# Optimization experiments

Hardware: AMD Instinct MI355X
Metric: run time of the kernel (lower is better)

## Reference

```python
import jax, jax.numpy as jnp
import numpy as np

B, N, D, C, H, W = 4, 900, 256, 256, 200, 200
HEADS, LVLS, PTS, K = 8, 1, 4, 10


def setup_inputs() -> dict:
    key = jax.random.key(0)
    ks = jax.random.split(key, 16)
    s = 0.02
    return {
        "query_embed": jax.random.normal(ks[0], (B, N, D), jnp.float32),
        "ctrl_points": jax.random.uniform(ks[1], (B, N, 4, 2), jnp.float32, -50.0, 50.0),
        "bev_features": jax.random.normal(ks[2], (B, C, H, W), jnp.float32),
        "spatial_shapes": jnp.array([[H, W]], dtype=jnp.int32),
        "pc_range": jnp.array([-51.2, -51.2, -5.0, 51.2, 51.2, 3.0], jnp.float32),
        "Wq": s * jax.random.normal(ks[3], (D, D)), "bq": jnp.zeros((D,)),
        "Wv": s * jax.random.normal(ks[4], (C, D)), "bv": jnp.zeros((D,)),
        "Woff": s * jax.random.normal(ks[5], (D, HEADS * LVLS * PTS * 2)), "boff": jnp.zeros((HEADS * LVLS * PTS * 2,)),
        "Wattn": s * jax.random.normal(ks[6], (D, HEADS * LVLS * PTS)), "battn": jnp.zeros((HEADS * LVLS * PTS,)),
        "Wmo": s * jax.random.normal(ks[7], (D, D)), "bmo": jnp.zeros((D,)),
        "Wo": s * jax.random.normal(ks[8], (D, D)), "bo": jnp.zeros((D,)),
    }


def _forward(query_embed, ctrl_points, bev_features, spatial_shapes, pc_range,
             Wq, bq, Wv, bv, Woff, boff, Wattn, battn, Wmo, bmo, Wo, bo):
    b, n, d = query_embed.shape
    _, c, h, w = bev_features.shape
    hd = d // HEADS

    # --- cubic Bezier interpolation: (B,N,4,2) -> (B,N,K,2) dense points ---
    t = jnp.linspace(0.0, 1.0, K, dtype=query_embed.dtype)
    basis = jnp.stack([(1 - t) ** 3, 3 * (1 - t) ** 2 * t, 3 * (1 - t) * t ** 2, t ** 3], axis=-1)  # (K,4)
    dense = jnp.einsum('kc,bncd->bnkd', basis, ctrl_points)
    # --- normalize to [0,1] by pc_range, clamp to [0.01,0.99] ---
    nx = (dense[..., 0] - pc_range[0]) / (pc_range[3] - pc_range[0])
    ny = (dense[..., 1] - pc_range[1]) / (pc_range[4] - pc_range[1])
    ref = jnp.clip(jnp.stack([nx, ny], axis=-1), 0.01, 0.99)  # (B,N,K,2)

    # --- projections ---
    q = query_embed @ Wq + bq                                       # (B,N,D) (identity for residual)
    v = bev_features.reshape(b, c, h * w).transpose(0, 2, 1) @ Wv + bv  # (B,HW,D)
    v = v.reshape(b, h * w, HEADS, hd)

    off = (q @ Woff + boff).reshape(b, n, HEADS, LVLS, PTS, 2)
    aw = jax.nn.softmax((q @ Wattn + battn).reshape(b, n, HEADS, LVLS * PTS), axis=-1)
    aw = aw.reshape(b, n, HEADS, PTS)  # LVLS == 1

    # offset normalizer = (W, H) per level
    normalizer = jnp.stack([spatial_shapes[..., 1], spatial_shapes[..., 0]], axis=-1).astype(q.dtype)  # (L,2)
    # sampling locations: broadcast K bezier points against heads/points offsets
    loc = ref[:, :, None, :, None, :] + off / normalizer[None, None, None, :, None, :]  # (B,N,HEADS,K,PTS,2)

    # --- bilinear sampling, align_corners=False, zero padding ---
    gx = loc[..., 0] * w - 0.5
    gy = loc[..., 1] * h - 0.5
    x0 = jnp.floor(gx)
    y0 = jnp.floor(gy)
    wx = gx - x0
    wy = gy - y0
    x0i = x0.astype(jnp.int32)
    y0i = y0.astype(jnp.int32)

    vflat = v.transpose(0, 2, 1, 3).reshape(b * HEADS, h * w, hd)  # (B*HEADS, HW, hd)

    def flat(a):  # (B,N,HEADS,K,PTS) -> (B*HEADS, N*K*PTS)
        return a.transpose(0, 2, 1, 3, 4).reshape(b * HEADS, n * K * PTS)

    acc = jnp.zeros((b * HEADS, n * K * PTS, hd), dtype=q.dtype)
    for dx, dy in ((0, 0), (1, 0), (0, 1), (1, 1)):
        ix = flat(x0i) + dx
        iy = flat(y0i) + dy
        wxx = flat(wx) if dx else (1.0 - flat(wx))
        wyy = flat(wy) if dy else (1.0 - flat(wy))
        valid = (ix >= 0) & (ix < w) & (iy >= 0) & (iy < h)
        idx = jnp.clip(iy, 0, h - 1) * w + jnp.clip(ix, 0, w - 1)
        corner = jnp.take_along_axis(vflat, idx[..., None], axis=1)  # (B*HEADS, Npts, hd)
        acc = acc + corner * (wxx * wyy * valid.astype(q.dtype))[..., None]

    sampled = acc.reshape(b, HEADS, n, K, PTS, hd)
    # weighted sum over (K, PTS); attention weights shared across the K bezier points
    out = jnp.einsum('bhnkpd,bnhp->bnhd', sampled, aw).reshape(b, n, d)
    out = out @ Wmo + bmo + q   # mmcv MSDeformAttn output_proj + residual (identity = query)
    out = out @ Wo + bo         # outer output_proj
    return out


def reference(query_embed, ctrl_points, bev_features, spatial_shapes, pc_range,
              Wq, bq, Wv, bv, Woff, boff, Wattn, battn, Wmo, bmo, Wo, bo):
    return _forward(query_embed, ctrl_points, bev_features, spatial_shapes, pc_range,
                    Wq, bq, Wv, bv, Woff, boff, Wattn, battn, Wmo, bmo, Wo, bo)
```

## Files before the change

kernel.cpp:

```cpp
#include <hip/hip_runtime.h>
#include <hip/hip_bf16.h>
#include <math.h>


typedef unsigned short u16;
typedef unsigned int u32;
typedef short bf16x8 __attribute__((ext_vector_type(8)));
typedef float f32x4 __attribute__((ext_vector_type(4)));

__device__ __forceinline__ float bflo(u32 w) {
  union { u32 i; float f; } c; c.i = w << 16; return c.f;
}
__device__ __forceinline__ float bfhi(u32 w) {
  union { u32 i; float f; } c; c.i = w & 0xffff0000u; return c.f;
}
__device__ __forceinline__ u16 f2bf(float f) {
  union { float f; u32 i; } c; c.f = f;
  u32 u = c.i;
  return (u16)((u + 0x7FFFu + ((u >> 16) & 1u)) >> 16);
}
__device__ __forceinline__ int imin(int a, int b) { return a < b ? a : b; }
__device__ __forceinline__ int imax(int a, int b) { return a > b ? a : b; }

__device__ __forceinline__ void glds16(const u16* g, u16* l) {
  __builtin_amdgcn_global_load_lds(
      (__attribute__((address_space(1))) const void*)g,
      (__attribute__((address_space(3))) void*)l, 16, 0, 0);
}

__global__ __launch_bounds__(256) void prep_weights(
    const float* __restrict__ Wq, const float* __restrict__ Wv,
    const float* __restrict__ Woff, const float* __restrict__ Wattn,
    const float* __restrict__ Wmo, const float* __restrict__ Wo,
    const float* __restrict__ bq, const float* __restrict__ boff,
    const float* __restrict__ battn, const float* __restrict__ bmo,
    const float* __restrict__ bo, const float* __restrict__ query,
    u16* __restrict__ bqoaT, u16* __restrict__ wvT, u16* __restrict__ woCat,
    float* __restrict__ bcat, float* __restrict__ bprime,
    u16* __restrict__ qin)
{
  const int idx = blockIdx.x * 256 + threadIdx.x;
  {
    int i = idx * 4;
    float4 v = *(const float4*)(query + i);
    uint2 st;
    st.x = (u32)f2bf(v.x) | ((u32)f2bf(v.y) << 16);
    st.y = (u32)f2bf(v.z) | ((u32)f2bf(v.w) << 16);
    *(uint2*)(qin + i) = st;
  }
  if (idx < 65536) {
    int r = idx >> 8, c = idx & 255;
    bqoaT[idx] = f2bf(Wq[c * 256 + r]);
    wvT[idx]   = f2bf(Wv[c * 256 + r]);
  }
  if (idx < 24576) {
    int n = idx >> 8, k = idx & 255;
    const float* wq = Wq + k * 256;
    float s = 0.f;
    if (n < 64) {
      const float* wo = Woff + n;
#pragma unroll 4
      for (int c = 0; c < 256; c += 4) {
        float4 a = *(const float4*)(wq + c);
        s += a.x * wo[(c + 0) * 64] + a.y * wo[(c + 1) * 64] +
             a.z * wo[(c + 2) * 64] + a.w * wo[(c + 3) * 64];
      }
    } else {
      const float* wa = Wattn + (n - 64);
#pragma unroll 4
      for (int c = 0; c < 256; c += 4) {
        float4 a = *(const float4*)(wq + c);
        s += a.x * wa[(c + 0) * 32] + a.y * wa[(c + 1) * 32] +
             a.z * wa[(c + 2) * 32] + a.w * wa[(c + 3) * 32];
      }
    }
    bqoaT[65536 + idx] = f2bf(s);
  }
  if (idx < 131072) {
    int n = idx >> 9, k = idx & 511;
    float s;
    if (k >= 256) {
      s = Wo[(size_t)(k - 256) * 256 + n];
    } else {
      const float* wm = Wmo + k * 256;
      const float* wo = Wo + n;
      s = 0.f;
#pragma unroll 4
      for (int c = 0; c < 256; c += 4) {
        float4 a = *(const float4*)(wm + c);
        s += a.x * wo[(c + 0) * 256] + a.y * wo[(c + 1) * 256] +
             a.z * wo[(c + 2) * 256] + a.w * wo[(c + 3) * 256];
      }
    }
    woCat[idx] = f2bf(s);
  }
  if (idx >= 131072 && idx < 131328) {
    int n = idx - 131072;
    const float* wo = Wo + n;
    float s = bo[n];
    for (int c = 0; c < 256; ++c) s += bmo[c] * wo[c * 256];
    bprime[n] = s;
  }
  if (idx >= 131328 && idx < 131680) {
    int n = idx - 131328;
    if (n < 256) {
      bcat[n] = bq[n];
    } else {
      int j = n - 256;
      float s;
      if (j < 64) {
        const float* wo = Woff + j;
        s = boff[j];
        for (int c = 0; c < 256; ++c) s += bq[c] * wo[c * 64];
      } else {
        const float* wa = Wattn + (j - 64);
        s = battn[j - 64];
        for (int c = 0; c < 256; ++c) s += bq[c] * wa[c * 32];
      }
      bcat[n] = s;
    }
  }
}

enum { GM_F32 = 0, GM_SPLIT = 1 };

template <int MODE>
__global__ __launch_bounds__(256) void gemm_bt(
    const u16* __restrict__ A, const u16* __restrict__ Bt,
    const float* __restrict__ bias,
    u16* __restrict__ outb, float* __restrict__ outf,
    int M, int N, int K, int lda, int ldo)
{
  __shared__ __align__(16) u16 lA[128 * 32];
  __shared__ __align__(16) u16 lB[128 * 32];
  const int tid = threadIdx.x;
  const int wv = tid >> 6, lane = tid & 63;
  const int m0 = blockIdx.y * 128;
  const int n0 = blockIdx.x * 128;

  const int crow = lane >> 2;
  const int ckoff = (lane & 3) * 8;
  const int a1 = imin(m0 + wv * 16 + crow, M - 1);
  const int a2 = imin(m0 + (wv + 4) * 16 + crow, M - 1);
  const int b1 = imin(n0 + wv * 16 + crow, N - 1);
  const int b2 = imin(n0 + (wv + 4) * 16 + crow, N - 1);
  const u16* gA1 = A + (size_t)a1 * lda + ckoff;
  const u16* gA2 = A + (size_t)a2 * lda + ckoff;
  const u16* gB1 = Bt + (size_t)b1 * K + ckoff;
  const u16* gB2 = Bt + (size_t)b2 * K + ckoff;
  u16* lA1 = lA + wv * 512;  u16* lA2 = lA + (wv + 4) * 512;
  u16* lB1 = lB + wv * 512;  u16* lB2 = lB + (wv + 4) * 512;

  const int fm = (wv & 1) * 64, fn = (wv >> 1) * 64;
  const int fr = lane & 15, fk = (lane >> 4) * 8;

  f32x4 acc[4][4];
#pragma unroll
  for (int i = 0; i < 4; ++i)
#pragma unroll
    for (int j = 0; j < 4; ++j) acc[i][j] = (f32x4){0.f, 0.f, 0.f, 0.f};

  for (int k0 = 0; k0 < K; k0 += 32) {
    glds16(gA1 + k0, lA1);
    glds16(gA2 + k0, lA2);
    glds16(gB1 + k0, lB1);
    glds16(gB2 + k0, lB2);
    __syncthreads();
    bf16x8 af[4], bfv[4];
#pragma unroll
    for (int i = 0; i < 4; ++i)
      af[i] = *(const bf16x8*)&lA[(fm + i * 16 + fr) * 32 + fk];
#pragma unroll
    for (int j = 0; j < 4; ++j)
      bfv[j] = *(const bf16x8*)&lB[(fn + j * 16 + fr) * 32 + fk];
    __syncthreads();
#pragma unroll
    for (int i = 0; i < 4; ++i)
#pragma unroll
      for (int j = 0; j < 4; ++j)
        acc[i][j] = __builtin_amdgcn_mfma_f32_16x16x32_bf16(af[i], bfv[j], acc[i][j], 0, 0, 0);
  }

  const int quad = lane >> 4;
#pragma unroll
  for (int j = 0; j < 4; ++j) {
    const int n = n0 + fn + j * 16 + fr;
    const bool nok = (n < N);
    const float bcol = bias[nok ? n : 0];
#pragma unroll
    for (int i = 0; i < 4; ++i) {
      const int mb = m0 + fm + i * 16 + quad * 4;
#pragma unroll
      for (int r = 0; r < 4; ++r) {
        const int m = mb + r;
        if (m < M && nok) {
          float x = acc[i][j][r] + bcol;
          if (MODE == GM_F32) {
            outf[(size_t)m * ldo + n] = x;
          } else {
            if (n < 256) outb[(size_t)m * 512 + n] = f2bf(x);
            else outf[(size_t)m * 96 + (n - 256)] = x;
          }
        }
      }
    }
  }
}

#define LOADB(S, R0, R1, R2, R3)                                   \
  { const float* s2_ = src + (size_t)((S) * 32) * 40000;           \
    R0 = *(const float4*)(s2_);                                    \
    R1 = *(const float4*)(s2_ + 4);                                \
    R2 = *(const float4*)(s2_ + 40000);                            \
    R3 = *(const float4*)(s2_ + 40004); }

#define CVW8(BUF, R0, R1, R2, R3)                                            \
  { u32* lbw_ = (u32*)(BUF); u32 pk_;                                        \
    asm("v_cvt_pk_bf16_f32 %0, %1, %2" : "=v"(pk_) : "v"(R0.x), "v"(R2.x)); \
    lbw_[(wrow + 0) * 16 + wslot] = pk_;                                     \
    asm("v_cvt_pk_bf16_f32 %0, %1, %2" : "=v"(pk_) : "v"(R0.y), "v"(R2.y)); \
    lbw_[(wrow + 1) * 16 + wslot] = pk_;                                     \
    asm("v_cvt_pk_bf16_f32 %0, %1, %2" : "=v"(pk_) : "v"(R0.z), "v"(R2.z)); \
    lbw_[(wrow + 2) * 16 + wslot] = pk_;                                     \
    asm("v_cvt_pk_bf16_f32 %0, %1, %2" : "=v"(pk_) : "v"(R0.w), "v"(R2.w)); \
    lbw_[(wrow + 3) * 16 + wslot] = pk_;                                     \
    asm("v_cvt_pk_bf16_f32 %0, %1, %2" : "=v"(pk_) : "v"(R1.x), "v"(R3.x)); \
    lbw_[(wrow + 4) * 16 + wslot] = pk_;                                     \
    asm("v_cvt_pk_bf16_f32 %0, %1, %2" : "=v"(pk_) : "v"(R1.y), "v"(R3.y)); \
    lbw_[(wrow + 5) * 16 + wslot] = pk_;                                     \
    asm("v_cvt_pk_bf16_f32 %0, %1, %2" : "=v"(pk_) : "v"(R1.z), "v"(R3.z)); \
    lbw_[(wrow + 6) * 16 + wslot] = pk_;                                     \
    asm("v_cvt_pk_bf16_f32 %0, %1, %2" : "=v"(pk_) : "v"(R1.w), "v"(R3.w)); \
    lbw_[(wrow + 7) * 16 + wslot] = pk_; }

__global__ __launch_bounds__(256, 2) void gemm_v(
    const u16* __restrict__ A,
    const float* __restrict__ bev,
    const float* __restrict__ bias,
    u16* __restrict__ outb)
{
  __shared__ __align__(16) u16 lA[8 * 128 * 32];
  __shared__ __align__(16) u16 lB[2][128 * 32];
  const int tid = threadIdx.x;
  const int wv = tid >> 6, lane = tid & 63;
  const int m0 = blockIdx.x * 128;
  const int n0 = blockIdx.y * 128;
  const int z = blockIdx.z;

  const int crow = lane >> 2, ckoff = (lane & 3) * 8;
  const u16* gA1 = A + (size_t)(m0 + wv * 16 + crow) * 256 + ckoff;
  const u16* gA2 = A + (size_t)(m0 + (wv + 4) * 16 + crow) * 256 + ckoff;
  u16* lA1 = lA + wv * 512;
  u16* lA2 = lA + (wv + 4) * 512;

  const int kp = tid >> 4, nb = tid & 15;
  const int cb = imin(n0 + nb * 8, 40000 - 8);
  const float* src = bev + ((size_t)z * 256 + 2 * kp) * 40000 + cb;
  const int wslot = (((kp >> 2) ^ (nb & 3)) << 2) + (kp & 3);
  const int wrow = nb * 8;

  const int fm = (wv & 1) * 64, fn = (wv >> 1) * 64;
  const int fr = lane & 15, fk = (lane >> 4) * 8;

  f32x4 acc[4][4];
#pragma unroll
  for (int i = 0; i < 4; ++i)
#pragma unroll
    for (int j = 0; j < 4; ++j) acc[i][j] = (f32x4){0.f, 0.f, 0.f, 0.f};

  float4 ra0, ra1, ra2, ra3, rb0, rb1, rb2, rb3;

  LOADB(0, ra0, ra1, ra2, ra3);
#pragma unroll
  for (int s = 0; s < 8; ++s) {
    glds16(gA1 + s * 32, lA1 + s * 4096);
    glds16(gA2 + s * 32, lA2 + s * 4096);
  }
  asm volatile("" ::: "memory");
  CVW8(lB[0], ra0, ra1, ra2, ra3);
  asm volatile("" ::: "memory");
  LOADB(1, rb0, rb1, rb2, rb3);
  __builtin_amdgcn_sched_barrier(0);
  asm volatile("s_waitcnt vmcnt(4) lgkmcnt(0)" ::: "memory");
  __builtin_amdgcn_sched_barrier(0);
  __builtin_amdgcn_s_barrier();
  __builtin_amdgcn_sched_barrier(0);

#pragma unroll
  for (int t = 0; t < 8; ++t) {
    bf16x8 af[4], bfv[4];
#pragma unroll
    for (int i = 0; i < 4; ++i)
      af[i] = *(const bf16x8*)&lA[t * 4096 + (fm + i * 16 + fr) * 32 + fk];
#pragma unroll
    for (int j = 0; j < 4; ++j) {
      const int n = fn + j * 16 + fr;
      const int pc = (((lane >> 4) ^ ((n >> 3) & 3)) << 3);
      bfv[j] = *(const bf16x8*)&lB[t & 1][n * 32 + pc];
    }
    if (t < 7) {
      if ((t & 1) == 0) { CVW8(lB[1], rb0, rb1, rb2, rb3); }
      else              { CVW8(lB[0], ra0, ra1, ra2, ra3); }
    }
    if (t < 6) {
      if ((t & 1) == 0) { LOADB(t + 2, ra0, ra1, ra2, ra3); }
      else              { LOADB(t + 2, rb0, rb1, rb2, rb3); }
    }
#pragma unroll
    for (int i = 0; i < 4; ++i)
#pragma unroll
      for (int j = 0; j < 4; ++j)
        acc[i][j] = __builtin_amdgcn_mfma_f32_16x16x32_bf16(af[i], bfv[j], acc[i][j], 0, 0, 0);
    if (t < 7) {
      __builtin_amdgcn_sched_barrier(0);
      asm volatile("s_waitcnt lgkmcnt(0)" ::: "memory");
      __builtin_amdgcn_sched_barrier(0);
      __builtin_amdgcn_s_barrier();
      __builtin_amdgcn_sched_barrier(0);
    }
  }

  const int quad = lane >> 4;
#pragma unroll
  for (int j = 0; j < 4; ++j) {
    const int n = n0 + fn + j * 16 + fr;
    if (n < 40000) {
#pragma unroll
      for (int i = 0; i < 4; ++i) {
        const int mb = m0 + fm + i * 16 + quad * 4;
        u16 u0 = f2bf(acc[i][j][0] + bias[mb + 0]);
        u16 u1 = f2bf(acc[i][j][1] + bias[mb + 1]);
        u16 u2 = f2bf(acc[i][j][2] + bias[mb + 2]);
        u16 u3 = f2bf(acc[i][j][3] + bias[mb + 3]);
        size_t off = (size_t)z * (8ull * 40000 * 32) +
                     (size_t)(mb >> 5) * (40000 * 32) + (size_t)n * 32 + (mb & 31);
        uint2 st; st.x = (u32)u0 | ((u32)u1 << 16); st.y = (u32)u2 | ((u32)u3 << 16);
        *(uint2*)(outb + off) = st;
      }
    }
  }
}

__global__ __launch_bounds__(256) void sampler(
    const float* __restrict__ ctrl,
    const float* __restrict__ pc,
    const float* __restrict__ oa_,
    const u16* __restrict__ v,
    u16* __restrict__ attn_out)
{
  __shared__ int   sX0[4][40], sY0[4][40];
  __shared__ float sWx[4][40], sWy[4][40], sAw[4][40];
  const int w = threadIdx.x >> 6, lane = threadIdx.x & 63;
  const int bh = blockIdx.x & 31;
  const int n = (blockIdx.x >> 5) * 4 + w;
  const int h = bh & 7, b = bh >> 3;
  const int row = b * 900 + n;

  if (lane < 40) {
    const int k = lane >> 2, p = lane & 3;
    const float t = (float)k * (1.0f / 9.0f), u = 1.f - t;
    const float c0 = u * u * u, c1 = 3.f * u * u * t, c2 = 3.f * u * t * t, c3 = t * t * t;
    const float* cp = ctrl + (size_t)row * 8;
    float cx = c0 * cp[0] + c1 * cp[2] + c2 * cp[4] + c3 * cp[6];
    float cy = c0 * cp[1] + c1 * cp[3] + c2 * cp[5] + c3 * cp[7];
    float nx = (cx - pc[0]) / (pc[3] - pc[0]);
    float ny = (cy - pc[1]) / (pc[4] - pc[1]);
    nx = fminf(fmaxf(nx, 0.01f), 0.99f);
    ny = fminf(fmaxf(ny, 0.01f), 0.99f);
    const float* oa = oa_ + (size_t)row * 96;
    float ox = oa[h * 8 + p * 2 + 0], oy = oa[h * 8 + p * 2 + 1];
    float l0 = oa[64 + h * 4 + 0], l1 = oa[64 + h * 4 + 1];
    float l2 = oa[64 + h * 4 + 2], l3 = oa[64 + h * 4 + 3];
    float mx = fmaxf(fmaxf(l0, l1), fmaxf(l2, l3));
    float e0 = __expf(l0 - mx), e1 = __expf(l1 - mx), e2 = __expf(l2 - mx), e3 = __expf(l3 - mx);
    float lp = (p == 0) ? l0 : (p == 1) ? l1 : (p == 2) ? l2 : l3;
    float aw = __expf(lp - mx) / (e0 + e1 + e2 + e3);
    float gx = (nx + ox * (1.f / 200.f)) * 200.f - 0.5f;
    float gy = (ny + oy * (1.f / 200.f)) * 200.f - 0.5f;
    float x0 = floorf(gx), y0 = floorf(gy);
    sX0[w][lane] = (int)x0; sY0[w][lane] = (int)y0;
    sWx[w][lane] = gx - x0; sWy[w][lane] = gy - y0; sAw[w][lane] = aw;
  }
  __syncthreads();

  const int sg = lane >> 3;
  const int ch0 = (lane & 7) * 4;
  const u16* vb = v + ((size_t)(b * 8 + h)) * (40000 * 32) + ch0;
  float a0 = 0.f, a1 = 0.f, a2 = 0.f, a3 = 0.f;
#pragma unroll
  for (int p = 0; p < 5; ++p) {
    const int s = p * 8 + sg;
    const int x0 = sX0[w][s], y0 = sY0[w][s];
    const float wx = sWx[w][s], wy = sWy[w][s], aw = sAw[w][s];
    const int x1 = x0 + 1, y1 = y0 + 1;
    const int cx0 = imin(imax(x0, 0), 199), cx1 = imin(imax(x1, 0), 199);
    const int cy0 = imin(imax(y0, 0), 199), cy1 = imin(imax(y1, 0), 199);
    const bool vx0 = (u32)x0 < 200u, vx1 = (u32)x1 < 200u;
    const bool vy0 = (u32)y0 < 200u, vy1 = (u32)y1 < 200u;
    const float w00 = (vx0 && vy0) ? aw * (1.f - wx) * (1.f - wy) : 0.f;
    const float w10 = (vx1 && vy0) ? aw * wx * (1.f - wy) : 0.f;
    const float w01 = (vx0 && vy1) ? aw * (1.f - wx) * wy : 0.f;
    const float w11 = (vx1 && vy1) ? aw * wx * wy : 0.f;
    uint2 d00 = *(const uint2*)(vb + (size_t)(cy0 * 200 + cx0) * 32);
    uint2 d10 = *(const uint2*)(vb + (size_t)(cy0 * 200 + cx1) * 32);
    uint2 d01 = *(const uint2*)(vb + (size_t)(cy1 * 200 + cx0) * 32);
    uint2 d11 = *(const uint2*)(vb + (size_t)(cy1 * 200 + cx1) * 32);
    a0 += w00 * bflo(d00.x) + w10 * bflo(d10.x) + w01 * bflo(d01.x) + w11 * bflo(d11.x);
    a1 += w00 * bfhi(d00.x) + w10 * bfhi(d10.x) + w01 * bfhi(d01.x) + w11 * bfhi(d11.x);
    a2 += w00 * bflo(d00.y) + w10 * bflo(d10.y) + w01 * bflo(d01.y) + w11 * bflo(d11.y);
    a3 += w00 * bfhi(d00.y) + w10 * bfhi(d10.y) + w01 * bfhi(d01.y) + w11 * bfhi(d11.y);
  }
#pragma unroll
  for (int off = 8; off < 64; off <<= 1) {
    a0 += __shfl_xor(a0, off);
    a1 += __shfl_xor(a1, off);
    a2 += __shfl_xor(a2, off);
    a3 += __shfl_xor(a3, off);
  }
  if (lane < 8) {
    uint2 st;
    st.x = (u32)f2bf(a0) | ((u32)f2bf(a1) << 16);
    st.y = (u32)f2bf(a2) | ((u32)f2bf(a3) << 16);
    *(uint2*)(attn_out + (size_t)row * 512 + h * 32 + ch0) = st;
  }
}

extern "C" void kernel_launch(void* const* d_in, const int* in_sizes, int n_in,
                              void* d_out, int out_size, void* d_ws, size_t ws_size,
                              hipStream_t stream)
{
  const float* query = (const float*)d_in[0];
  const float* ctrl  = (const float*)d_in[1];
  const float* bev   = (const float*)d_in[2];
  const float* pc    = (const float*)d_in[4];
  const float* Wq    = (const float*)d_in[5];  const float* bq    = (const float*)d_in[6];
  const float* Wv    = (const float*)d_in[7];  const float* bv    = (const float*)d_in[8];
  const float* Woff  = (const float*)d_in[9];  const float* boff  = (const float*)d_in[10];
  const float* Wattn = (const float*)d_in[11]; const float* battn = (const float*)d_in[12];
  const float* Wmo   = (const float*)d_in[13]; const float* bmo   = (const float*)d_in[14];
  const float* Wo    = (const float*)d_in[15]; const float* bo    = (const float*)d_in[16];

  char* ws = (char*)d_ws;
  size_t off = 0;
  auto alloc = [&](size_t bytes) -> void* {
    void* p = ws + off; off += (bytes + 255) & ~(size_t)255; return p;
  };
  u16*  v     = (u16*)alloc(4ull * 8 * 40000 * 32 * 2);
  u16*  qin   = (u16*)alloc(3600ull * 256 * 2);
  u16*  wvT   = (u16*)alloc(65536 * 2);
  u16*  bqoaT = (u16*)alloc(352 * 256 * 2);
  u16*  woCat = (u16*)alloc(256 * 512 * 2);
  float* bcat = (float*)alloc(352 * 4);
  float* bprime = (float*)alloc(256 * 4);
  float* oaf  = (float*)alloc(3600ull * 96 * 4);
  u16*  qcat  = (u16*)alloc(3600ull * 512 * 2);
  (void)ws_size; (void)in_sizes; (void)n_in; (void)out_size;

  prep_weights<<<900, 256, 0, stream>>>(Wq, Wv, Woff, Wattn, Wmo, Wo,
                                        bq, boff, battn, bmo, bo, query,
                                        bqoaT, wvT, woCat, bcat, bprime, qin);
  gemm_v<<<dim3(2, 313, 4), 256, 0, stream>>>(wvT, bev, bv, v);
  gemm_bt<GM_SPLIT><<<dim3(3, 29), 256, 0, stream>>>(
      qin, bqoaT, bcat, qcat + 256, oaf, 3600, 352, 256, 256, 0);
  sampler<<<7200, 256, 0, stream>>>(ctrl, pc, oaf, v, qcat);
  gemm_bt<GM_F32><<<dim3(2, 29), 256, 0, stream>>>(
      qcat, woCat, bprime, nullptr, (float*)d_out, 3600, 256, 512, 512, 256);
}
```

Baseline: 376.2 us.

## Deepen bev register prefetch to four stages and add LDS XOR swizzle

The V-projection GEMM now keeps four register stages of fp32 BEV loads in flight instead of two, issuing stages 1-3 up front and refilling them during the first four k-steps. This hides more global-memory latency on the strided BEV reads. It also adds an extra XOR bit (on nb bit 2 / n bit 5) to the LDS write and read addresses for the B tile, meant to cut bank conflicts. The explicit vmcnt wait is replaced by __syncthreads. The cost is roughly double the VGPRs for prefetch buffers, which may reduce occupancy under launch_bounds(256,2).

Result: slower. 384.0 us (+2.1%).

```diff
diff --git a/kernel.cpp b/kernel.cpp
--- a/kernel.cpp
+++ b/kernel.cpp
@@ -217,21 +217,21 @@
 #define CVW8(BUF, R0, R1, R2, R3)                                            \
   { u32* lbw_ = (u32*)(BUF); u32 pk_;                                        \
     asm("v_cvt_pk_bf16_f32 %0, %1, %2" : "=v"(pk_) : "v"(R0.x), "v"(R2.x)); \
-    lbw_[(wrow + 0) * 16 + wslot] = pk_;                                     \
+    lbw_[(((wrow + 0) * 16 + wslot) ^ wxor)] = pk_;                          \
     asm("v_cvt_pk_bf16_f32 %0, %1, %2" : "=v"(pk_) : "v"(R0.y), "v"(R2.y)); \
-    lbw_[(wrow + 1) * 16 + wslot] = pk_;                                     \
+    lbw_[(((wrow + 1) * 16 + wslot) ^ wxor)] = pk_;                          \
     asm("v_cvt_pk_bf16_f32 %0, %1, %2" : "=v"(pk_) : "v"(R0.z), "v"(R2.z)); \
-    lbw_[(wrow + 2) * 16 + wslot] = pk_;                                     \
+    lbw_[(((wrow + 2) * 16 + wslot) ^ wxor)] = pk_;                          \
     asm("v_cvt_pk_bf16_f32 %0, %1, %2" : "=v"(pk_) : "v"(R0.w), "v"(R2.w)); \
-    lbw_[(wrow + 3) * 16 + wslot] = pk_;                                     \
+    lbw_[(((wrow + 3) * 16 + wslot) ^ wxor)] = pk_;                          \
     asm("v_cvt_pk_bf16_f32 %0, %1, %2" : "=v"(pk_) : "v"(R1.x), "v"(R3.x)); \
-    lbw_[(wrow + 4) * 16 + wslot] = pk_;                                     \
+    lbw_[(((wrow + 4) * 16 + wslot) ^ wxor)] = pk_;                          \
     asm("v_cvt_pk_bf16_f32 %0, %1, %2" : "=v"(pk_) : "v"(R1.y), "v"(R3.y)); \
-    lbw_[(wrow + 5) * 16 + wslot] = pk_;                                     \
+    lbw_[(((wrow + 5) * 16 + wslot) ^ wxor)] = pk_;                          \
     asm("v_cvt_pk_bf16_f32 %0, %1, %2" : "=v"(pk_) : "v"(R1.z), "v"(R3.z)); \
-    lbw_[(wrow + 6) * 16 + wslot] = pk_;                                     \
+    lbw_[(((wrow + 6) * 16 + wslot) ^ wxor)] = pk_;                          \
     asm("v_cvt_pk_bf16_f32 %0, %1, %2" : "=v"(pk_) : "v"(R1.w), "v"(R3.w)); \
-    lbw_[(wrow + 7) * 16 + wslot] = pk_; }
+    lbw_[(((wrow + 7) * 16 + wslot) ^ wxor)] = pk_; }
 
 __global__ __launch_bounds__(256, 2) void gemm_v(
     const u16* __restrict__ A,
@@ -257,6 +257,7 @@
   const int cb = imin(n0 + nb * 8, 40000 - 8);
   const float* src = bev + ((size_t)z * 256 + 2 * kp) * 40000 + cb;
   const int wslot = (((kp >> 2) ^ (nb & 3)) << 2) + (kp & 3);
+  const int wxor = ((nb >> 2) & 1) << 4;
   const int wrow = nb * 8;
 
   const int fm = (wv & 1) * 64, fn = (wv >> 1) * 64;
@@ -268,23 +269,21 @@
 #pragma unroll
     for (int j = 0; j < 4; ++j) acc[i][j] = (f32x4){0.f, 0.f, 0.f, 0.f};
 
-  float4 ra0, ra1, ra2, ra3, rb0, rb1, rb2, rb3;
-
-  LOADB(0, ra0, ra1, ra2, ra3);
+  float4 s0a, s0b, s0c, s0d, s1a, s1b, s1c, s1d;
+  float4 s2a, s2b, s2c, s2d, s3a, s3b, s3c, s3d;
+
+  LOADB(0, s0a, s0b, s0c, s0d);
 #pragma unroll
   for (int s = 0; s < 8; ++s) {
     glds16(gA1 + s * 32, lA1 + s * 4096);
     glds16(gA2 + s * 32, lA2 + s * 4096);
   }
+  LOADB(1, s1a, s1b, s1c, s1d);
+  LOADB(2, s2a, s2b, s2c, s2d);
+  LOADB(3, s3a, s3b, s3c, s3d);
   asm volatile("" ::: "memory");
-  CVW8(lB[0], ra0, ra1, ra2, ra3);
-  asm volatile("" ::: "memory");
-  LOADB(1, rb0, rb1, rb2, rb3);
-  __builtin_amdgcn_sched_barrier(0);
-  asm volatile("s_waitcnt vmcnt(4) lgkmcnt(0)" ::: "memory");
-  __builtin_amdgcn_sched_barrier(0);
-  __builtin_amdgcn_s_barrier();
-  __builtin_amdgcn_sched_barrier(0);
+  CVW8(lB[0], s0a, s0b, s0c, s0d);
+  __syncthreads();
 
 #pragma unroll
   for (int t = 0; t < 8; ++t) {
@@ -296,16 +295,20 @@
     for (int j = 0; j < 4; ++j) {
       const int n = fn + j * 16 + fr;
       const int pc = (((lane >> 4) ^ ((n >> 3) & 3)) << 3);
-      bfv[j] = *(const bf16x8*)&lB[t & 1][n * 32 + pc];
-    }
-    if (t < 7) {
-      if ((t & 1) == 0) { CVW8(lB[1], rb0, rb1, rb2, rb3); }
-      else              { CVW8(lB[0], ra0, ra1, ra2, ra3); }
-    }
-    if (t < 6) {
-      if ((t & 1) == 0) { LOADB(t + 2, ra0, ra1, ra2, ra3); }
-      else              { LOADB(t + 2, rb0, rb1, rb2, rb3); }
-    }
+      const int ri = (n * 32 + pc) ^ (((n >> 5) & 1) << 5);
+      bfv[j] = *(const bf16x8*)&lB[t & 1][ri];
+    }
+    if (t == 0)      { LOADB(4, s0a, s0b, s0c, s0d); }
+    else if (t == 1) { LOADB(5, s1a, s1b, s1c, s1d); }
+    else if (t == 2) { LOADB(6, s2a, s2b, s2c, s2d); }
+    else if (t == 3) { LOADB(7, s3a, s3b, s3c, s3d); }
+    if (t == 0)      { CVW8(lB[1], s1a, s1b, s1c, s1d); }
+    else if (t == 1) { CVW8(lB[0], s2a, s2b, s2c, s2d); }
+    else if (t == 2) { CVW8(lB[1], s3a, s3b, s3c, s3d); }
+    else if (t == 3) { CVW8(lB[0], s0a, s0b, s0c, s0d); }
+    else if (t == 4) { CVW8(lB[1], s1a, s1b, s1c, s1d); }
+    else if (t == 5) { CVW8(lB[0], s2a, s2b, s2c, s2d); }
+    else if (t == 6) { CVW8(lB[1], s3a, s3b, s3c, s3d); }
 #pragma unroll
     for (int i = 0; i < 4; ++i)
 #pragma unroll
```
